# Kernel tuning notes

Hardware: AMD Instinct MI355X
Metric: run time of the kernel (lower is better)

Reference implementation:

```python
import jax, jax.numpy as jnp
import numpy as np

B_BOX = 2          # boxes per cell
C_CLS = 20         # classes
LAMBDA_COORD = 5.0
LAMBDA_NOOBJ = 0.5
N_EL = B_BOX * 5 + C_CLS  # 30


def setup_inputs() -> dict:
    key = jax.random.key(0)
    k1, k2, k3 = jax.random.split(key, 3)
    batch, S = 16384, 7
    pred = jax.random.normal(k1, (batch, S * S * N_EL), dtype=jnp.float32)
    tgt = jax.random.uniform(k2, (batch, S, S, N_EL), dtype=jnp.float32)
    obj = jax.random.uniform(k3, (batch, S, S)) > 0.7
    tgt = tgt.at[..., 5].set(jnp.where(obj, tgt[..., 5], 0.0))
    return {"pred_tensor": pred, "target_tensor": tgt}


def _pairwise_iou(p, t):
    # p, t: [..., B, 4] corner-format boxes (x1,y1,x2,y2)
    # returns iou[..., i, j] = IoU(pred_i, target_j)
    lt = jnp.maximum(p[..., :, None, :2], t[..., None, :, :2])
    rb = jnp.minimum(p[..., :, None, 2:4], t[..., None, :, 2:4])
    wh = jnp.clip(rb - lt, 0.0)
    inter = wh[..., 0] * wh[..., 1]
    a1 = (p[..., 2] - p[..., 0]) * (p[..., 3] - p[..., 1])
    a2 = (t[..., 2] - t[..., 0]) * (t[..., 3] - t[..., 1])
    denom = a1[..., :, None] + a2[..., None, :] - inter
    return inter / (denom + 1e-10)


def reference(pred_tensor, target_tensor):
    batch = target_tensor.shape[0]
    t = target_tensor.reshape(batch, -1, N_EL)   # [B, N, 30]
    p = pred_tensor.reshape(batch, -1, N_EL)
    coord = (t[..., 5] > 0)                      # object cells   [B, N]
    noobj = (t[..., 5] == 0)                     # no-object cells

    conf_idx = jnp.array([b * 5 + 4 for b in range(B_BOX)])
    # noobj: MSE on confidences only (sum reduction)
    d_conf = p[..., conf_idx] - t[..., conf_idx]
    noobj_loss = jnp.sum(noobj[..., None] * d_conf * d_conf)

    # class loss over object cells
    d_cls = p[..., 5 * B_BOX:] - t[..., 5 * B_BOX:]
    class_loss = jnp.sum(coord[..., None] * d_cls * d_cls)

    pb = p[..., :5 * B_BOX].reshape(batch, -1, B_BOX, 5)  # [B, N, Bx, 5]
    tb = t[..., :5 * B_BOX].reshape(batch, -1, B_BOX, 5)

    # responsible-box assignment: for each target box j, pred box argmax_i iou
    iou = _pairwise_iou(pb, tb)                  # [B, N, Bx_pred, Bx_tgt]
    max_idx = jnp.argmax(iou, axis=-2)           # [B, N, Bx_tgt] -> pred index
    resp = jnp.any(max_idx[..., None] == jnp.arange(B_BOX), axis=-2)  # [B, N, Bx]
    resp = resp & coord[..., None]
    rm = resp.astype(pb.dtype)

    d_c = pb[..., 4] - tb[..., 4]
    contain_loss = jnp.sum(rm * d_c * d_c)
    d_box = pb[..., :4] - tb[..., :4]
    loc_loss = jnp.sum(rm[..., None] * d_box * d_box)

    return (LAMBDA_COORD * loc_loss + contain_loss
            + LAMBDA_NOOBJ * noobj_loss + class_loss)
```

## Files before the change

### kernel.cpp

```cpp
#include <hip/hip_runtime.h>

#define N_EL 30
#define LAMBDA_COORD 5.0f
#define LAMBDA_NOOBJ 0.5f
#define CPB 256
#define FLOATS_PER (CPB * N_EL)
#define VEC4_PER (FLOATS_PER / 4)

typedef const __attribute__((address_space(1))) void gas_void;
typedef __attribute__((address_space(3))) void las_void;

__device__ __forceinline__ float iou_fn(const float* p, const float* t) {
    float ltx = fmaxf(p[0], t[0]);
    float lty = fmaxf(p[1], t[1]);
    float rbx = fminf(p[2], t[2]);
    float rby = fminf(p[3], t[3]);
    float w = fmaxf(rbx - ltx, 0.0f);
    float h = fmaxf(rby - lty, 0.0f);
    float inter = w * h;
    float a1 = (p[2] - p[0]) * (p[3] - p[1]);
    float a2 = (t[2] - t[0]) * (t[3] - t[1]);
    return inter / (a1 + a2 - inter + 1e-10f);
}

__global__ __launch_bounds__(256) void yolo_loss_main(
    const float* __restrict__ pred,
    const float* __restrict__ tgt,
    float* __restrict__ partials)
{
    __shared__ float sp[FLOATS_PER];
    __shared__ float st[FLOATS_PER];

    const int tid  = threadIdx.x;
    const int lane = tid & 63;
    const int wid  = tid >> 6;

    const float4* Pg = reinterpret_cast<const float4*>(pred) + (size_t)blockIdx.x * VEC4_PER;
    const float4* Tg = reinterpret_cast<const float4*>(tgt)  + (size_t)blockIdx.x * VEC4_PER;
    float4* sp4 = reinterpret_cast<float4*>(sp);
    float4* st4 = reinterpret_cast<float4*>(st);

    #pragma unroll
    for (int r = 0; r < 7; ++r) {
        int i     = r * 256 + tid;
        int wbase = r * 256 + (wid << 6);
        __builtin_amdgcn_global_load_lds((gas_void*)(Pg + i), (las_void*)(sp4 + wbase), 16, 0, 0);
        __builtin_amdgcn_global_load_lds((gas_void*)(Tg + i), (las_void*)(st4 + wbase), 16, 0, 0);
    }
    if (wid < 2) {
        int i     = 7 * 256 + tid;
        int wbase = 7 * 256 + (wid << 6);
        __builtin_amdgcn_global_load_lds((gas_void*)(Pg + i), (las_void*)(sp4 + wbase), 16, 0, 0);
        __builtin_amdgcn_global_load_lds((gas_void*)(Tg + i), (las_void*)(st4 + wbase), 16, 0, 0);
    }
    __syncthreads();

    float p[N_EL], t[N_EL];
    const float2* lp = reinterpret_cast<const float2*>(sp + tid * N_EL);
    const float2* lt = reinterpret_cast<const float2*>(st + tid * N_EL);
    #pragma unroll
    for (int i = 0; i < 15; ++i) {
        float2 a = lp[i]; p[2*i] = a.x; p[2*i+1] = a.y;
        float2 b = lt[i]; t[2*i] = b.x; t[2*i+1] = b.y;
    }

    bool coord = (t[5] > 0.0f);
    bool noobj = (t[5] == 0.0f);

    float d4 = p[4] - t[4];
    float d9 = p[9] - t[9];
    float noobj_loss = noobj ? (d4 * d4 + d9 * d9) : 0.0f;

    float cls = 0.0f;
    #pragma unroll
    for (int k = 10; k < 30; ++k) { float d = p[k] - t[k]; cls += d * d; }
    cls = coord ? cls : 0.0f;

    float iou00 = iou_fn(p,     t);
    float iou01 = iou_fn(p,     t + 5);
    float iou10 = iou_fn(p + 5, t);
    float iou11 = iou_fn(p + 5, t + 5);
    bool m0 = (iou10 > iou00);
    bool m1 = (iou11 > iou01);
    bool r0 = coord && ((!m0) || (!m1));
    bool r1 = coord && (m0 || m1);

    float contain = (r0 ? d4 * d4 : 0.0f) + (r1 ? d9 * d9 : 0.0f);

    float loc = 0.0f;
    #pragma unroll
    for (int k = 0; k < 4; ++k) { float d = p[k] - t[k]; loc += r0 ? d * d : 0.0f; }
    #pragma unroll
    for (int k = 5; k < 9; ++k) { float d = p[k] - t[k]; loc += r1 ? d * d : 0.0f; }

    float total = LAMBDA_COORD * loc + contain + LAMBDA_NOOBJ * noobj_loss + cls;

    #pragma unroll
    for (int off = 32; off > 0; off >>= 1)
        total += __shfl_down(total, off, 64);

    __shared__ float ws[4];
    if (lane == 0) ws[wid] = total;
    __syncthreads();
    if (tid == 0) {
        partials[blockIdx.x] = ws[0] + ws[1] + ws[2] + ws[3];
    }
}

__global__ __launch_bounds__(256) void yolo_loss_final(
    const float* __restrict__ partials,
    float* __restrict__ out,
    int n)
{
    const int tid = threadIdx.x;
    float s = 0.0f;
    for (int i = tid; i < n; i += 256) s += partials[i];

    #pragma unroll
    for (int off = 32; off > 0; off >>= 1)
        s += __shfl_down(s, off, 64);

    __shared__ float ws[4];
    int lane = tid & 63;
    int wid  = tid >> 6;
    if (lane == 0) ws[wid] = s;
    __syncthreads();
    if (tid == 0) out[0] = ws[0] + ws[1] + ws[2] + ws[3];
}

extern "C" void kernel_launch(void* const* d_in, const int* in_sizes, int n_in,
                              void* d_out, int out_size, void* d_ws, size_t ws_size,
                              hipStream_t stream) {
    const float* pred = (const float*)d_in[0];
    const float* tgt  = (const float*)d_in[1];
    float* out = (float*)d_out;
    float* partials = (float*)d_ws;
    int n_cells = in_sizes[0] / N_EL;
    int grid = n_cells / CPB;

    yolo_loss_main<<<grid, 256, 0, stream>>>(pred, tgt, partials);
    yolo_loss_final<<<1, 256, 0, stream>>>(partials, out, grid);
}
```

Before: 37.23 us.

## Use single-wave 64-cell blocks and vectorize the partial-sum reduction

Each block now holds one 64-thread wave covering 64 cells, which quadruples the grid and removes the cross-wave LDS reduction and second barrier. The partial tail load uses ordinary loads split between the pred and target buffers. The final reduction reads partials as float4. More, smaller blocks give finer-grained occupancy and less LDS per block, at the cost of four times as many partial writes and more block-launch overhead.

```diff
diff --git a/kernel.cpp b/kernel.cpp
--- a/kernel.cpp
+++ b/kernel.cpp
@@ -3,7 +3,7 @@
 #define N_EL 30
 #define LAMBDA_COORD 5.0f
 #define LAMBDA_NOOBJ 0.5f
-#define CPB 256
+#define CPB 64
 #define FLOATS_PER (CPB * N_EL)
 #define VEC4_PER (FLOATS_PER / 4)
 
@@ -23,7 +23,7 @@
     return inter / (a1 + a2 - inter + 1e-10f);
 }
 
-__global__ __launch_bounds__(256) void yolo_loss_main(
+__global__ __launch_bounds__(64) void yolo_loss_main(
     const float* __restrict__ pred,
     const float* __restrict__ tgt,
     float* __restrict__ partials)
@@ -31,9 +31,7 @@
     __shared__ float sp[FLOATS_PER];
     __shared__ float st[FLOATS_PER];
 
-    const int tid  = threadIdx.x;
-    const int lane = tid & 63;
-    const int wid  = tid >> 6;
+    const int lane = threadIdx.x;
 
     const float4* Pg = reinterpret_cast<const float4*>(pred) + (size_t)blockIdx.x * VEC4_PER;
     const float4* Tg = reinterpret_cast<const float4*>(tgt)  + (size_t)blockIdx.x * VEC4_PER;
@@ -42,22 +40,20 @@
 
     #pragma unroll
     for (int r = 0; r < 7; ++r) {
-        int i     = r * 256 + tid;
-        int wbase = r * 256 + (wid << 6);
-        __builtin_amdgcn_global_load_lds((gas_void*)(Pg + i), (las_void*)(sp4 + wbase), 16, 0, 0);
-        __builtin_amdgcn_global_load_lds((gas_void*)(Tg + i), (las_void*)(st4 + wbase), 16, 0, 0);
+        int i = r * 64 + lane;
+        __builtin_amdgcn_global_load_lds((gas_void*)(Pg + i), (las_void*)(sp4 + r * 64), 16, 0, 0);
+        __builtin_amdgcn_global_load_lds((gas_void*)(Tg + i), (las_void*)(st4 + r * 64), 16, 0, 0);
     }
-    if (wid < 2) {
-        int i     = 7 * 256 + tid;
-        int wbase = 7 * 256 + (wid << 6);
-        __builtin_amdgcn_global_load_lds((gas_void*)(Pg + i), (las_void*)(sp4 + wbase), 16, 0, 0);
-        __builtin_amdgcn_global_load_lds((gas_void*)(Tg + i), (las_void*)(st4 + wbase), 16, 0, 0);
+    {
+        int i = 7 * 64 + (lane & 31);
+        if (lane < 32) sp4[i] = Pg[i];
+        else           st4[i] = Tg[i];
     }
     __syncthreads();
 
     float p[N_EL], t[N_EL];
-    const float2* lp = reinterpret_cast<const float2*>(sp + tid * N_EL);
-    const float2* lt = reinterpret_cast<const float2*>(st + tid * N_EL);
+    const float2* lp = reinterpret_cast<const float2*>(sp + lane * N_EL);
+    const float2* lt = reinterpret_cast<const float2*>(st + lane * N_EL);
     #pragma unroll
     for (int i = 0; i < 15; ++i) {
         float2 a = lp[i]; p[2*i] = a.x; p[2*i+1] = a.y;
@@ -98,23 +94,21 @@
     #pragma unroll
     for (int off = 32; off > 0; off >>= 1)
         total += __shfl_down(total, off, 64);
-
-    __shared__ float ws[4];
-    if (lane == 0) ws[wid] = total;
-    __syncthreads();
-    if (tid == 0) {
-        partials[blockIdx.x] = ws[0] + ws[1] + ws[2] + ws[3];
-    }
+    if (lane == 0) partials[blockIdx.x] = total;
 }
 
 __global__ __launch_bounds__(256) void yolo_loss_final(
     const float* __restrict__ partials,
     float* __restrict__ out,
-    int n)
+    int n4)
 {
     const int tid = threadIdx.x;
+    const float4* p4 = reinterpret_cast<const float4*>(partials);
     float s = 0.0f;
-    for (int i = tid; i < n; i += 256) s += partials[i];
+    for (int i = tid; i < n4; i += 256) {
+        float4 v = p4[i];
+        s += v.x + v.y + v.z + v.w;
+    }
 
     #pragma unroll
     for (int off = 32; off > 0; off >>= 1)
@@ -138,6 +132,6 @@
     int n_cells = in_sizes[0] / N_EL;
     int grid = n_cells / CPB;
 
-    yolo_loss_main<<<grid, 256, 0, stream>>>(pred, tgt, partials);
-    yolo_loss_final<<<1, 256, 0, stream>>>(partials, out, grid);
+    yolo_loss_main<<<grid, 64, 0, stream>>>(pred, tgt, partials);
+    yolo_loss_final<<<1, 256, 0, stream>>>(partials, out, grid / 4);
 }
```

Result: slower. 38.29 us (+2.9%).
